# Optimization experiments

Measured on AMD Instinct MI355X. Metric: run time of the kernel, lower is better.

The kernel has to match this reference:

```python
import jax, jax.numpy as jnp
import numpy as np

G, IN_D, OUT_D, KQ_D = 8192, 512, 512, 128
EPS = 1e-12  # torch F.normalize default eps


def setup_inputs() -> dict:
    key = jax.random.key(0)
    ks = jax.random.split(key, 7)
    s_in = 1.0 / np.sqrt(IN_D)
    return {
        "x": jax.random.normal(ks[0], (G, IN_D), dtype=jnp.float32),
        "Wk": jax.random.uniform(ks[1], (KQ_D, IN_D), jnp.float32, -s_in, s_in),
        "bk": jax.random.uniform(ks[2], (KQ_D,), jnp.float32, -s_in, s_in),
        "Wq": jax.random.uniform(ks[3], (KQ_D, IN_D), jnp.float32, -s_in, s_in),
        "bq": jax.random.uniform(ks[4], (KQ_D,), jnp.float32, -s_in, s_in),
        "Wv": jax.random.uniform(ks[5], (OUT_D, IN_D), jnp.float32, -s_in, s_in),
        "bv": jax.random.uniform(ks[6], (OUT_D,), jnp.float32, -s_in, s_in),
    }


def reference(x, Wk, bk, Wq, bq, Wv, bv):
    # QKV projections (torch Linear: x @ W^T + b)
    k = x @ Wk.T + bk            # [g, kq]
    q = x @ Wq.T + bq            # [g, kq]
    v = x @ Wv.T + bv            # [g, outD]
    # g x g attention scores
    scores = k @ q.T             # [g, g]
    # L2-normalize each row (F.normalize with dim=-1): x / max(||x||_2, eps)
    norm = jnp.sqrt(jnp.sum(scores * scores, axis=-1, keepdims=True))
    scores_n = scores / jnp.maximum(norm, EPS)
    # value matmul + residual
    return scores_n @ v + v      # [g, outD]
```

## Files before the change

kernel.cpp:

```cpp
#include <hip/hip_runtime.h>
#include <hip/hip_bf16.h>
#include <stdint.h>

typedef __attribute__((ext_vector_type(8))) short bf16x8;
typedef __attribute__((ext_vector_type(4))) float f32x4;

__device__ __forceinline__ unsigned short f2bf(float f) {
  union { float f; uint32_t u; } v; v.f = f;
  uint32_t u = v.u;
  return (unsigned short)((u + 0x7fffu + ((u >> 16) & 1u)) >> 16);
}
__device__ __forceinline__ float bf2f(unsigned short h) {
  union { uint32_t u; float f; } v; v.u = ((uint32_t)h) << 16;
  return v.f;
}

#define GLL(g, l) __builtin_amdgcn_global_load_lds( \
    (const __attribute__((address_space(1))) void*)(g), \
    (__attribute__((address_space(3))) void*)(l), 16, 0, 0)
#define WAITV(N) asm volatile("s_waitcnt vmcnt(" #N ")" ::: "memory")
#define SFENCE() __builtin_amdgcn_sched_barrier(0)
#define RBAR()   __builtin_amdgcn_s_barrier()

__global__ void cvt_all(const float* __restrict__ x,
                        const float* __restrict__ wk, const float* __restrict__ wq,
                        const float* __restrict__ wv,
                        unsigned short* __restrict__ xb, unsigned short* __restrict__ wb) {
  const int i = (blockIdx.x * 256 + threadIdx.x) * 4;
  const float* src; unsigned short* dst; int off;
  if (i < 4194304) { src = x; dst = xb; off = i; }
  else {
    const int j = i - 4194304;
    if (j < 65536)       { src = wk; off = j; }
    else if (j < 131072) { src = wq; off = j - 65536; }
    else                 { src = wv; off = j - 131072; }
    dst = wb + (j - off);
  }
  const float4 v = *(const float4*)(src + off);
  ushort4 o; o.x = f2bf(v.x); o.y = f2bf(v.y); o.z = f2bf(v.z); o.w = f2bf(v.w);
  *(ushort4*)(dst + off) = o;
}

__global__ __launch_bounds__(256, 3) void qkv_gemm(
    const unsigned short* __restrict__ xb, const unsigned short* __restrict__ wb,
    const float* __restrict__ pbk, const float* __restrict__ pbq, const float* __restrict__ pbv,
    unsigned short* __restrict__ kb, unsigned short* __restrict__ qtb,
    unsigned short* __restrict__ vb, unsigned short* __restrict__ vtb)
{
  __shared__ unsigned short Alds[2][64 * 64];
  __shared__ unsigned short Blds[2][128 * 64];
  const int tid = threadIdx.x;
  const int lane = tid & 63;
  const int wid = tid >> 6;
  const int wm = wid >> 1, wn = wid & 1;
  const int wg = blockIdx.x;
  const int s = (wg & 7) * 96 + (wg >> 3);
  const int bx = s & 127, by = s >> 7;
  const int m0 = bx * 64, n0 = by * 128;
  const int l15 = lane & 15, l4 = lane >> 4;

  f32x4 acc[2][4] = {};

  auto stage = [&](int b, int kt) {
    const int k0 = kt * 64;
    #pragma unroll
    for (int p = 0; p < 2; ++p) {
      const int e = p * 256 + tid;
      const int row = e >> 3;
      const int cs = (e & 7) ^ (row & 7);
      GLL(xb + (size_t)(m0 + row) * 512 + k0 + cs * 8, &Alds[b][(p * 256 + (tid & ~63)) * 8]);
    }
    #pragma unroll
    for (int p = 0; p < 4; ++p) {
      const int e = p * 256 + tid;
      const int row = e >> 3;
      const int cs = (e & 7) ^ (row & 7);
      GLL(wb + (size_t)(n0 + row) * 512 + k0 + cs * 8, &Blds[b][(p * 256 + (tid & ~63)) * 8]);
    }
  };

  stage(0, 0);
  stage(1, 1);

  for (int kt = 0; kt < 8; ++kt) {
    const int cur = kt & 1;
    if (kt < 7) { WAITV(6); } else { WAITV(0); }
    RBAR();
    SFENCE();
    #pragma unroll
    for (int kk = 0; kk < 2; ++kk) {
      bf16x8 af[2], bfv[4];
      #pragma unroll
      for (int i = 0; i < 2; ++i) {
        const int ra = wm * 32 + i * 16 + l15;
        const int c  = kk * 4 + l4;
        af[i] = *(const bf16x8*)(&Alds[cur][ra * 64 + ((c ^ (ra & 7)) * 8)]);
      }
      #pragma unroll
      for (int j = 0; j < 4; ++j) {
        const int rb = wn * 64 + j * 16 + l15;
        const int c  = kk * 4 + l4;
        bfv[j] = *(const bf16x8*)(&Blds[cur][rb * 64 + ((c ^ (rb & 7)) * 8)]);
      }
      #pragma unroll
      for (int i = 0; i < 2; ++i)
        #pragma unroll
        for (int j = 0; j < 4; ++j)
          acc[i][j] = __builtin_amdgcn_mfma_f32_16x16x32_bf16(af[i], bfv[j], acc[i][j], 0, 0, 0);
    }
    SFENCE();
    RBAR();
    if (kt < 6) stage(cur, kt + 2);
  }

  #pragma unroll
  for (int i = 0; i < 2; ++i) {
    #pragma unroll
    for (int j = 0; j < 4; ++j) {
      const int rbase = m0 + wm * 32 + i * 16 + l4 * 4;
      const int c = n0 + wn * 64 + j * 16 + l15;
      const float bias = (c < 128) ? pbk[c] : (c < 256) ? pbq[c - 128] : pbv[c - 256];
      unsigned short o[4];
      #pragma unroll
      for (int r = 0; r < 4; ++r) o[r] = f2bf(acc[i][j][r] + bias);
      if (c < 128) {
        #pragma unroll
        for (int r = 0; r < 4; ++r) kb[(size_t)(rbase + r) * 128 + c] = o[r];
      } else if (c < 256) {
        ushort4 t; t.x = o[0]; t.y = o[1]; t.z = o[2]; t.w = o[3];
        *(ushort4*)(qtb + (size_t)(c - 128) * 8192 + rbase) = t;
      } else {
        const int vcol = c - 256;
        #pragma unroll
        for (int r = 0; r < 4; ++r) vb[(size_t)(rbase + r) * 512 + vcol] = o[r];
        ushort4 t; t.x = o[0]; t.y = o[1]; t.z = o[2]; t.w = o[3];
        *(ushort4*)(vtb + (size_t)vcol * 8192 + rbase) = t;
      }
    }
  }
}

__global__ __launch_bounds__(512) void gh_gemm(
    const unsigned short* __restrict__ qtb, const unsigned short* __restrict__ vtb,
    unsigned short* __restrict__ pb)
{
  __shared__ unsigned short Alds[2][128 * 64];
  __shared__ unsigned short Blds[2][80 * 64];
  const int tid = threadIdx.x, lane = tid & 63, wid = tid >> 6;
  const int l15 = lane & 15, l4 = lane >> 4;
  const int kc = blockIdx.x, nq = blockIdx.y;
  const int g0 = kc * 256;
  const int m0 = wid * 16;

  f32x4 acc[5] = {};

  auto stage = [&](int b, int st) {
    const int gs = g0 + st * 64;
    #pragma unroll
    for (int p = 0; p < 2; ++p) {
      const int e = p * 512 + tid;
      const int row = e >> 3;
      const int cs = (e & 7) ^ (row & 7);
      GLL(qtb + (size_t)row * 8192 + gs + cs * 8, &Alds[b][(p * 512 + (tid & ~63)) * 8]);
    }
    {
      const int row = tid >> 3;
      const int cglob = nq * 80 + row;
      const unsigned short* src = (cglob < 128) ? (qtb + (size_t)cglob * 8192)
                                                : (vtb + (size_t)(cglob - 128) * 8192);
      const int cs = (tid & 7) ^ (row & 7);
      GLL(src + gs + cs * 8, &Blds[b][(tid & ~63) * 8]);
    }
    if (tid < 128) {
      const int e = 512 + tid;
      const int row = e >> 3;
      const int cglob = nq * 80 + row;
      const unsigned short* src = (cglob < 128) ? (qtb + (size_t)cglob * 8192)
                                                : (vtb + (size_t)(cglob - 128) * 8192);
      const int cs = (e & 7) ^ (row & 7);
      GLL(src + gs + cs * 8, &Blds[b][(512 + (tid & ~63)) * 8]);
    }
  };

  stage(0, 0);
  stage(1, 1);

  for (int st = 0; st < 4; ++st) {
    const int cur = st & 1;
    if (st < 3) { WAITV(3); } else { WAITV(0); }
    RBAR();
    SFENCE();
    #pragma unroll
    for (int ks = 0; ks < 2; ++ks) {
      const int ra = m0 + l15;
      const int ca = ks * 4 + l4;
      const bf16x8 af = *(const bf16x8*)(&Alds[cur][ra * 64 + ((ca ^ (ra & 7)) * 8)]);
      #pragma unroll
      for (int nf = 0; nf < 5; ++nf) {
        const int rb = nf * 16 + l15;
        const bf16x8 bf = *(const bf16x8*)(&Blds[cur][rb * 64 + ((ca ^ (rb & 7)) * 8)]);
        acc[nf] = __builtin_amdgcn_mfma_f32_16x16x32_bf16(af, bf, acc[nf], 0, 0, 0);
      }
    }
    SFENCE();
    RBAR();
    if (st < 2) stage(cur, st + 2);
  }

  #pragma unroll
  for (int nf = 0; nf < 5; ++nf) {
    const int col = nq * 80 + nf * 16 + l15;
    #pragma unroll
    for (int r = 0; r < 4; ++r) {
      const int row = m0 + l4 * 4 + r;
      pb[((size_t)kc * 128 + row) * 640 + col] = f2bf(acc[nf][r]);
    }
  }
}

__global__ void gh_finalize(const unsigned short* __restrict__ pb,
                            unsigned short* __restrict__ Gb, unsigned short* __restrict__ Hbt) {
  const int idx = blockIdx.x * 256 + threadIdx.x;
  float s = 0.f;
  #pragma unroll
  for (int p = 0; p < 32; ++p) s += bf2f(pb[(size_t)p * 81920 + idx]);
  const int m = idx / 640, c = idx % 640;
  if (c < 128) Gb[m * 128 + c] = f2bf(s);
  else         Hbt[(size_t)(c - 128) * 128 + m] = f2bf(s);
}

__global__ __launch_bounds__(512, 2) void tnorm(
    const unsigned short* __restrict__ kb, const unsigned short* __restrict__ Gb,
    float* __restrict__ rnm)
{
  __shared__ unsigned short Kld[128 * 128];
  __shared__ unsigned short Gld[128 * 128];
  const int tid = threadIdx.x, lane = tid & 63, wid = tid >> 6;
  const int l15 = lane & 15, l4 = lane >> 4;
  const int m0 = blockIdx.x * 128;

  #pragma unroll
  for (int p = 0; p < 4; ++p) {
    const int e = p * 512 + tid;
    const int row = e >> 4, ch = e & 15;
    const int cs = ch ^ ((row & 7) << 1);
    GLL(kb + (size_t)(m0 + row) * 128 + cs * 8, &Kld[(e & ~63) * 8]);
    GLL(Gb + (size_t)row * 128 + cs * 8,        &Gld[(e & ~63) * 8]);
  }
  WAITV(0);
  __syncthreads();

  bf16x8 af[4];
  #pragma unroll
  for (int ks = 0; ks < 4; ++ks) {
    const int row = wid * 16 + l15, ci = ks * 4 + l4;
    af[ks] = *(const bf16x8*)((const char*)Kld + row * 256 + ((ci ^ ((row & 7) << 1)) * 16));
  }
  f32x4 tac[8] = {};
  #pragma unroll
  for (int ks = 0; ks < 4; ++ks) {
    #pragma unroll
    for (int nf = 0; nf < 8; ++nf) {
      const int grow = nf * 16 + l15, ci = ks * 4 + l4;
      const bf16x8 bf = *(const bf16x8*)((const char*)Gld + grow * 256 +
                                         ((ci ^ ((grow & 7) << 1)) * 16));
      tac[nf] = __builtin_amdgcn_mfma_f32_16x16x32_bf16(af[ks], bf, tac[nf], 0, 0, 0);
    }
  }

  float ssq[4] = {0.f, 0.f, 0.f, 0.f};
  #pragma unroll
  for (int nf = 0; nf < 8; ++nf) {
    #pragma unroll
    for (int r = 0; r < 4; ++r) {
      const int row = wid * 16 + l4 * 4 + r;
      const int col = nf * 16 + l15;
      const unsigned short kv = *(const unsigned short*)((const char*)Kld + row * 256 +
          ((((col >> 3)) ^ ((row & 7) << 1)) * 16) + (col & 7) * 2);
      ssq[r] += tac[nf][r] * bf2f(kv);
    }
  }
  #pragma unroll
  for (int d = 1; d < 16; d <<= 1)
    #pragma unroll
    for (int r = 0; r < 4; ++r) ssq[r] += __shfl_xor(ssq[r], d);
  if (l15 == 0) {
    #pragma unroll
    for (int r = 0; r < 4; ++r)
      rnm[m0 + wid * 16 + l4 * 4 + r] = 1.0f / fmaxf(sqrtf(ssq[r]), 1e-12f);
  }
}

__global__ __launch_bounds__(512, 4) void uv_out(
    const unsigned short* __restrict__ kb, const unsigned short* __restrict__ Hbt,
    const float* __restrict__ rnm, const unsigned short* __restrict__ vb,
    float* __restrict__ out)
{
  __shared__ unsigned short Kld[128 * 128];
  __shared__ unsigned short Hld[128 * 128];
  const int tid = threadIdx.x, lane = tid & 63, wid = tid >> 6;
  const int l15 = lane & 15, l4 = lane >> 4;
  const int m0 = blockIdx.x * 128, n0 = blockIdx.y * 128;
  const int wm = wid >> 2, wn = wid & 3;

  #pragma unroll
  for (int p = 0; p < 4; ++p) {
    const int e = p * 512 + tid;
    const int row = e >> 4, ch = e & 15;
    const int cs = ch ^ ((row & 7) << 1);
    GLL(kb  + (size_t)(m0 + row) * 128 + cs * 8, &Kld[(e & ~63) * 8]);
    GLL(Hbt + (size_t)(n0 + row) * 128 + cs * 8, &Hld[(e & ~63) * 8]);
  }
  WAITV(0);
  __syncthreads();

  f32x4 acc[4][2] = {};
  #pragma unroll
  for (int ks = 0; ks < 4; ++ks) {
    const int ci = ks * 4 + l4;
    bf16x8 af[4], bf[2];
    #pragma unroll
    for (int i = 0; i < 4; ++i) {
      const int row = wm * 64 + i * 16 + l15;
      af[i] = *(const bf16x8*)((const char*)Kld + row * 256 + ((ci ^ ((row & 7) << 1)) * 16));
    }
    #pragma unroll
    for (int j = 0; j < 2; ++j) {
      const int col = wn * 32 + j * 16 + l15;
      bf[j] = *(const bf16x8*)((const char*)Hld + col * 256 + ((ci ^ ((col & 7) << 1)) * 16));
    }
    #pragma unroll
    for (int i = 0; i < 4; ++i)
      #pragma unroll
      for (int j = 0; j < 2; ++j)
        acc[i][j] = __builtin_amdgcn_mfma_f32_16x16x32_bf16(af[i], bf[j], acc[i][j], 0, 0, 0);
  }

  #pragma unroll
  for (int i = 0; i < 4; ++i) {
    float rn[4];
    #pragma unroll
    for (int r = 0; r < 4; ++r) rn[r] = rnm[m0 + wm * 64 + i * 16 + l4 * 4 + r];
    #pragma unroll
    for (int j = 0; j < 2; ++j) {
      const int col = n0 + wn * 32 + j * 16 + l15;
      #pragma unroll
      for (int r = 0; r < 4; ++r) {
        const int row = m0 + wm * 64 + i * 16 + l4 * 4 + r;
        out[(size_t)row * 512 + col] =
            acc[i][j][r] * rn[r] + bf2f(vb[(size_t)row * 512 + col]);
      }
    }
  }
}

extern "C" void kernel_launch(void* const* d_in, const int* in_sizes, int n_in,
                              void* d_out, int out_size, void* d_ws, size_t ws_size,
                              hipStream_t stream) {
  const float* x  = (const float*)d_in[0];
  const float* Wk = (const float*)d_in[1];
  const float* bk = (const float*)d_in[2];
  const float* Wq = (const float*)d_in[3];
  const float* bq = (const float*)d_in[4];
  const float* Wv = (const float*)d_in[5];
  const float* bv = (const float*)d_in[6];
  float* out = (float*)d_out;

  char* ws = (char*)d_ws;
  unsigned short* xb   = (unsigned short*)(ws);
  unsigned short* wb   = (unsigned short*)(ws + 8388608);
  unsigned short* kb   = (unsigned short*)(ws + 9175040);
  unsigned short* vb   = (unsigned short*)(ws + 11272192);
  unsigned short* vtb  = (unsigned short*)(ws + 19660800);
  unsigned short* qtb  = (unsigned short*)(ws + 28049408);
  unsigned short* pb   = (unsigned short*)(ws + 30146560);
  unsigned short* Gb   = (unsigned short*)(ws + 35389440);
  unsigned short* Hbt  = (unsigned short*)(ws + 35422208);
  float*          rnm  = (float*)(ws + 35553280);

  cvt_all<<<4480, 256, 0, stream>>>(x, Wk, Wq, Wv, xb, wb);
  qkv_gemm<<<768, 256, 0, stream>>>(xb, wb, bk, bq, bv, kb, qtb, vb, vtb);
  gh_gemm<<<dim3(32, 8), 512, 0, stream>>>(qtb, vtb, pb);
  gh_finalize<<<320, 256, 0, stream>>>(pb, Gb, Hbt);
  tnorm<<<64, 512, 0, stream>>>(kb, Gb, rnm);
  uv_out<<<dim3(64, 4), 512, 0, stream>>>(kb, Hbt, rnm, vb, out);
}
```

Before: 47.65 us.

## Fuse row-norm into output GEMM and enlarge QKV GEMM tile to 128x128

```diff
diff --git a/kernel.cpp b/kernel.cpp
--- a/kernel.cpp
+++ b/kernel.cpp
@@ -41,40 +41,34 @@
   *(ushort4*)(dst + off) = o;
 }
 
-__global__ __launch_bounds__(256, 3) void qkv_gemm(
+__global__ __launch_bounds__(256, 2) void qkv_gemm(
     const unsigned short* __restrict__ xb, const unsigned short* __restrict__ wb,
     const float* __restrict__ pbk, const float* __restrict__ pbq, const float* __restrict__ pbv,
     unsigned short* __restrict__ kb, unsigned short* __restrict__ qtb,
     unsigned short* __restrict__ vb, unsigned short* __restrict__ vtb)
 {
-  __shared__ unsigned short Alds[2][64 * 64];
+  __shared__ unsigned short Alds[2][128 * 64];
   __shared__ unsigned short Blds[2][128 * 64];
   const int tid = threadIdx.x;
   const int lane = tid & 63;
   const int wid = tid >> 6;
   const int wm = wid >> 1, wn = wid & 1;
   const int wg = blockIdx.x;
-  const int s = (wg & 7) * 96 + (wg >> 3);
-  const int bx = s & 127, by = s >> 7;
-  const int m0 = bx * 64, n0 = by * 128;
+  const int s = (wg & 7) * 48 + (wg >> 3);
+  const int bx = s & 63, by = s >> 6;
+  const int m0 = bx * 128, n0 = by * 128;
   const int l15 = lane & 15, l4 = lane >> 4;
 
-  f32x4 acc[2][4] = {};
+  f32x4 acc[4][4] = {};
 
   auto stage = [&](int b, int kt) {
     const int k0 = kt * 64;
     #pragma unroll
-    for (int p = 0; p < 2; ++p) {
+    for (int p = 0; p < 4; ++p) {
       const int e = p * 256 + tid;
       const int row = e >> 3;
       const int cs = (e & 7) ^ (row & 7);
       GLL(xb + (size_t)(m0 + row) * 512 + k0 + cs * 8, &Alds[b][(p * 256 + (tid & ~63)) * 8]);
-    }
-    #pragma unroll
-    for (int p = 0; p < 4; ++p) {
-      const int e = p * 256 + tid;
-      const int row = e >> 3;
-      const int cs = (e & 7) ^ (row & 7);
       GLL(wb + (size_t)(n0 + row) * 512 + k0 + cs * 8, &Blds[b][(p * 256 + (tid & ~63)) * 8]);
     }
   };
@@ -84,26 +78,22 @@
 
   for (int kt = 0; kt < 8; ++kt) {
     const int cur = kt & 1;
-    if (kt < 7) { WAITV(6); } else { WAITV(0); }
+    if (kt < 7) { WAITV(8); } else { WAITV(0); }
     RBAR();
     SFENCE();
     #pragma unroll
     for (int kk = 0; kk < 2; ++kk) {
-      bf16x8 af[2], bfv[4];
-      #pragma unroll
-      for (int i = 0; i < 2; ++i) {
-        const int ra = wm * 32 + i * 16 + l15;
-        const int c  = kk * 4 + l4;
-        af[i] = *(const bf16x8*)(&Alds[cur][ra * 64 + ((c ^ (ra & 7)) * 8)]);
-      }
-      #pragma unroll
-      for (int j = 0; j < 4; ++j) {
-        const int rb = wn * 64 + j * 16 + l15;
-        const int c  = kk * 4 + l4;
-        bfv[j] = *(const bf16x8*)(&Blds[cur][rb * 64 + ((c ^ (rb & 7)) * 8)]);
-      }
-      #pragma unroll
-      for (int i = 0; i < 2; ++i)
+      bf16x8 af[4], bfv[4];
+      const int c = kk * 4 + l4;
+      #pragma unroll
+      for (int i = 0; i < 4; ++i) {
+        const int ra = wm * 64 + i * 16 + l15;
+        af[i]  = *(const bf16x8*)(&Alds[cur][ra * 64 + ((c ^ (ra & 7)) * 8)]);
+        const int rb = wn * 64 + i * 16 + l15;
+        bfv[i] = *(const bf16x8*)(&Blds[cur][rb * 64 + ((c ^ (rb & 7)) * 8)]);
+      }
+      #pragma unroll
+      for (int i = 0; i < 4; ++i)
         #pragma unroll
         for (int j = 0; j < 4; ++j)
           acc[i][j] = __builtin_amdgcn_mfma_f32_16x16x32_bf16(af[i], bfv[j], acc[i][j], 0, 0, 0);
@@ -114,10 +104,10 @@
   }
 
   #pragma unroll
-  for (int i = 0; i < 2; ++i) {
+  for (int i = 0; i < 4; ++i) {
     #pragma unroll
     for (int j = 0; j < 4; ++j) {
-      const int rbase = m0 + wm * 32 + i * 16 + l4 * 4;
+      const int rbase = m0 + wm * 64 + i * 16 + l4 * 4;
       const int c = n0 + wn * 64 + j * 16 + l15;
       const float bias = (c < 128) ? pbk[c] : (c < 256) ? pbq[c - 128] : pbv[c - 256];
       unsigned short o[4];
@@ -229,15 +219,19 @@
   else         Hbt[(size_t)(c - 128) * 128 + m] = f2bf(s);
 }
 
-__global__ __launch_bounds__(512, 2) void tnorm(
+__global__ __launch_bounds__(512, 2) void uvn_out(
     const unsigned short* __restrict__ kb, const unsigned short* __restrict__ Gb,
-    float* __restrict__ rnm)
+    const unsigned short* __restrict__ Hbt, const unsigned short* __restrict__ vb,
+    float* __restrict__ out)
 {
   __shared__ unsigned short Kld[128 * 128];
   __shared__ unsigned short Gld[128 * 128];
+  __shared__ unsigned short Hld[128 * 128];
+  __shared__ float rnm_lds[128];
   const int tid = threadIdx.x, lane = tid & 63, wid = tid >> 6;
   const int l15 = lane & 15, l4 = lane >> 4;
-  const int m0 = blockIdx.x * 128;
+  const int m0 = blockIdx.x * 128, n0 = blockIdx.y * 128;
+  const int wm = wid >> 2, wn = wid & 3;
 
   #pragma unroll
   for (int p = 0; p < 4; ++p) {
@@ -245,72 +239,66 @@
     const int row = e >> 4, ch = e & 15;
     const int cs = ch ^ ((row & 7) << 1);
     GLL(kb + (size_t)(m0 + row) * 128 + cs * 8, &Kld[(e & ~63) * 8]);
-    GLL(Gb + (size_t)row * 128 + cs * 8,        &Gld[(e & ~63) * 8]);
-  }
-  WAITV(0);
-  __syncthreads();
-
-  bf16x8 af[4];
-  #pragma unroll
-  for (int ks = 0; ks < 4; ++ks) {
-    const int row = wid * 16 + l15, ci = ks * 4 + l4;
-    af[ks] = *(const bf16x8*)((const char*)Kld + row * 256 + ((ci ^ ((row & 7) << 1)) * 16));
-  }
-  f32x4 tac[8] = {};
-  #pragma unroll
-  for (int ks = 0; ks < 4; ++ks) {
-    #pragma unroll
-    for (int nf = 0; nf < 8; ++nf) {
-      const int grow = nf * 16 + l15, ci = ks * 4 + l4;
-      const bf16x8 bf = *(const bf16x8*)((const char*)Gld + grow * 256 +
-                                         ((ci ^ ((grow & 7) << 1)) * 16));
-      tac[nf] = __builtin_amdgcn_mfma_f32_16x16x32_bf16(af[ks], bf, tac[nf], 0, 0, 0);
-    }
-  }
-
-  float ssq[4] = {0.f, 0.f, 0.f, 0.f};
-  #pragma unroll
-  for (int nf = 0; nf < 8; ++nf) {
-    #pragma unroll
-    for (int r = 0; r < 4; ++r) {
-      const int row = wid * 16 + l4 * 4 + r;
-      const int col = nf * 16 + l15;
-      const unsigned short kv = *(const unsigned short*)((const char*)Kld + row * 256 +
-          ((((col >> 3)) ^ ((row & 7) << 1)) * 16) + (col & 7) * 2);
-      ssq[r] += tac[nf][r] * bf2f(kv);
-    }
-  }
-  #pragma unroll
-  for (int d = 1; d < 16; d <<= 1)
-    #pragma unroll
-    for (int r = 0; r < 4; ++r) ssq[r] += __shfl_xor(ssq[r], d);
-  if (l15 == 0) {
-    #pragma unroll
-    for (int r = 0; r < 4; ++r)
-      rnm[m0 + wid * 16 + l4 * 4 + r] = 1.0f / fmaxf(sqrtf(ssq[r]), 1e-12f);
-  }
-}
-
-__global__ __launch_bounds__(512, 4) void uv_out(
-    const unsigned short* __restrict__ kb, const unsigned short* __restrict__ Hbt,
-    const float* __restrict__ rnm, const unsigned short* __restrict__ vb,
-    float* __restrict__ out)
-{
-  __shared__ unsigned short Kld[128 * 128];
-  __shared__ unsigned short Hld[128 * 128];
-  const int tid = threadIdx.x, lane = tid & 63, wid = tid >> 6;
-  const int l15 = lane & 15, l4 = lane >> 4;
-  const int m0 = blockIdx.x * 128, n0 = blockIdx.y * 128;
-  const int wm = wid >> 2, wn = wid & 3;
-
+  }
   #pragma unroll
   for (int p = 0; p < 4; ++p) {
     const int e = p * 512 + tid;
     const int row = e >> 4, ch = e & 15;
     const int cs = ch ^ ((row & 7) << 1);
-    GLL(kb  + (size_t)(m0 + row) * 128 + cs * 8, &Kld[(e & ~63) * 8]);
+    GLL(Gb + (size_t)row * 128 + cs * 8, &Gld[(e & ~63) * 8]);
+  }
+  #pragma unroll
+  for (int p = 0; p < 4; ++p) {
+    const int e = p * 512 + tid;
+    const int row = e >> 4, ch = e & 15;
+    const int cs = ch ^ ((row & 7) << 1);
     GLL(Hbt + (size_t)(n0 + row) * 128 + cs * 8, &Hld[(e & ~63) * 8]);
   }
+  WAITV(4);
+  __syncthreads();
+
+  {
+    bf16x8 afn[4];
+    #pragma unroll
+    for (int ks = 0; ks < 4; ++ks) {
+      const int row = wid * 16 + l15, ci = ks * 4 + l4;
+      afn[ks] = *(const bf16x8*)((const char*)Kld + row * 256 + ((ci ^ ((row & 7) << 1)) * 16));
+    }
+    f32x4 tac[8] = {};
+    #pragma unroll
+    for (int ks = 0; ks < 4; ++ks) {
+      const int ci = ks * 4 + l4;
+      #pragma unroll
+      for (int nf = 0; nf < 8; ++nf) {
+        const int grow = nf * 16 + l15;
+        const bf16x8 bf = *(const bf16x8*)((const char*)Gld + grow * 256 +
+                                           ((ci ^ ((grow & 7) << 1)) * 16));
+        tac[nf] = __builtin_amdgcn_mfma_f32_16x16x32_bf16(afn[ks], bf, tac[nf], 0, 0, 0);
+      }
+    }
+    float ssq[4] = {0.f, 0.f, 0.f, 0.f};
+    #pragma unroll
+    for (int nf = 0; nf < 8; ++nf) {
+      #pragma unroll
+      for (int r = 0; r < 4; ++r) {
+        const int row = wid * 16 + l4 * 4 + r;
+        const int col = nf * 16 + l15;
+        const unsigned short kv = *(const unsigned short*)((const char*)Kld + row * 256 +
+            (((col >> 3) ^ ((row & 7) << 1)) * 16) + (col & 7) * 2);
+        ssq[r] += tac[nf][r] * bf2f(kv);
+      }
+    }
+    #pragma unroll
+    for (int d = 1; d < 16; d <<= 1)
+      #pragma unroll
+      for (int r = 0; r < 4; ++r) ssq[r] += __shfl_xor(ssq[r], d);
+    if (l15 == 0) {
+      #pragma unroll
+      for (int r = 0; r < 4; ++r)
+        rnm_lds[wid * 16 + l4 * 4 + r] = 1.0f / fmaxf(sqrtf(ssq[r]), 1e-12f);
+    }
+  }
+
   WAITV(0);
   __syncthreads();
 
@@ -340,7 +328,7 @@
   for (int i = 0; i < 4; ++i) {
     float rn[4];
     #pragma unroll
-    for (int r = 0; r < 4; ++r) rn[r] = rnm[m0 + wm * 64 + i * 16 + l4 * 4 + r];
+    for (int r = 0; r < 4; ++r) rn[r] = rnm_lds[wm * 64 + i * 16 + l4 * 4 + r];
     #pragma unroll
     for (int j = 0; j < 2; ++j) {
       const int col = n0 + wn * 32 + j * 16 + l15;
@@ -376,12 +364,10 @@
   unsigned short* pb   = (unsigned short*)(ws + 30146560);
   unsigned short* Gb   = (unsigned short*)(ws + 35389440);
   unsigned short* Hbt  = (unsigned short*)(ws + 35422208);
-  float*          rnm  = (float*)(ws + 35553280);
 
   cvt_all<<<4480, 256, 0, stream>>>(x, Wk, Wq, Wv, xb, wb);
-  qkv_gemm<<<768, 256, 0, stream>>>(xb, wb, bk, bq, bv, kb, qtb, vb, vtb);
+  qkv_gemm<<<384, 256, 0, stream>>>(xb, wb, bk, bq, bv, kb, qtb, vb, vtb);
   gh_gemm<<<dim3(32, 8), 512, 0, stream>>>(qtb, vtb, pb);
   gh_finalize<<<320, 256, 0, stream>>>(pb, Gb, Hbt);
-  tnorm<<<64, 512, 0, stream>>>(kb, Gb, rnm);
-  uv_out<<<dim3(64, 4), 512, 0, stream>>>(kb, Hbt, rnm, vb, out);
-}
+  uvn_out<<<dim3(64, 4), 512, 0, stream>>>(kb, Gb, Hbt, vb, out);
+}
```

Measured after the change: 49.21 us. +3.3%, slower.
